# Kernel optimization log

Hardware: AMD Instinct MI355X
Metric: run time of the kernel (lower is better)

## Reference

```python
import jax, jax.numpy as jnp
import numpy as np

CUTOFFS = (2000, 20000, 50000)  # shortlist end, tail cluster boundaries; last == vocab
B, H, V = 8192, 1024, 50000
N_TAIL = len(CUTOFFS) - 1  # 2


def setup_inputs() -> dict:
    key = jax.random.key(0)
    ks = jax.random.split(key, 10)
    hidden = jax.random.normal(ks[0], (B, H), jnp.float32)
    targets = jax.random.randint(ks[1], (B,), 0, V, dtype=jnp.int64)
    embed_weight = jax.random.normal(ks[2], (V, H), jnp.float32) * 0.02
    # head: tail_vectors = nn.Linear(H, n_tail) -> W:(n_tail,H), b:(n_tail,)
    tail_vec_W = jax.random.normal(ks[3], (N_TAIL, H), jnp.float32) * 0.02
    tail_vec_b = jax.random.normal(ks[4], (N_TAIL,), jnp.float32) * 0.02
    shortlist_bias = jax.random.normal(ks[5], (CUTOFFS[0],), jnp.float32)
    bias0 = jax.random.normal(ks[6], (CUTOFFS[1] - CUTOFFS[0],), jnp.float32)
    bias1 = jax.random.normal(ks[7], (CUTOFFS[2] - CUTOFFS[1],), jnp.float32)
    # down_i = nn.Linear(H, H // 4**i, bias=False) -> W:(H//4**i, H)
    down0_W = jax.random.normal(ks[8], (H, H), jnp.float32) * (1.0 / np.sqrt(H))
    down1_W = jax.random.normal(ks[9], (H // 4, H), jnp.float32) * (1.0 / np.sqrt(H))
    return {
        "hidden": hidden, "embed_weight": embed_weight,
        "tail_vec_W": tail_vec_W, "tail_vec_b": tail_vec_b,
        "shortlist_bias": shortlist_bias, "bias0": bias0, "bias1": bias1,
        "down0_W": down0_W, "down1_W": down1_W, "targets": targets,
    }


def _cluster_ids(targets):
    # data-dependent sizes -> host-side index computation (matches torch nonzero)
    t = np.asarray(targets)
    ids = []
    for i in range(N_TAIL):
        ids.append(jnp.asarray(np.nonzero((t >= CUTOFFS[i]) & (t < CUTOFFS[i + 1]))[0]))
    return ids


def reference(hidden, embed_weight, tail_vec_W, tail_vec_b, shortlist_bias,
              bias0, bias1, down0_W, down1_W, targets):
    idx0, idx1 = _cluster_ids(targets)
    # head: shortlist logits + one logit per tail cluster
    shortlist = embed_weight[:CUTOFFS[0]]                       # (c0, H)
    head = jnp.concatenate(
        [hidden @ shortlist.T + shortlist_bias[None, :],         # (B, c0)
         hidden @ tail_vec_W.T + tail_vec_b[None, :]], axis=1)   # (B, n_tail)
    # tail cluster 0: down0 is H->H (reduce_factor**0 == 1, still applied)
    dec0 = embed_weight[CUTOFFS[0]:CUTOFFS[1]] @ down0_W.T       # (18000, H)
    out0 = (hidden[idx0] @ down0_W.T) @ dec0.T + bias0[None, :]  # (n0, 18000)
    # tail cluster 1: down1 is H -> H//4
    dec1 = embed_weight[CUTOFFS[1]:CUTOFFS[2]] @ down1_W.T       # (30000, 256)
    out1 = (hidden[idx1] @ down1_W.T) @ dec1.T + bias1[None, :]  # (n1, 30000)
    return (head, out0, out1)
```

## Files before the change

kernel.cpp:

```cpp
#include <hip/hip_runtime.h>
#include <hip/hip_bf16.h>

#define CUT0 2000
#define CUT1 20000
#define CUT2 50000
#define BSZ  8192
#define HDIM 1024
#define N0MAX 18000
#define N1MAX 30000
#define HEADW 2002

typedef __attribute__((ext_vector_type(8))) short bf16x8;
typedef __attribute__((ext_vector_type(4))) float f32x4;
typedef __attribute__((ext_vector_type(4))) unsigned short us4;

__device__ __forceinline__ unsigned short f2bf(float x) {
    unsigned u = __float_as_uint(x);
    unsigned r = u + 0x7fffu + ((u >> 16) & 1u);
    return (unsigned short)(r >> 16);
}

typedef const __attribute__((address_space(1))) void* gas_ptr;
typedef __attribute__((address_space(3))) void* las_ptr;

__device__ __forceinline__ void load_lds16(const void* g, void* l) {
    __builtin_amdgcn_global_load_lds((gas_ptr)g, (las_ptr)l, 16, 0, 0);
}

__global__ __launch_bounds__(1024) void build_idx(const int* __restrict__ targets,
                                                  int* __restrict__ n0,
                                                  int* __restrict__ n1,
                                                  int* __restrict__ idx0,
                                                  int* __restrict__ idx1) {
    __shared__ int s0[1024], s1[1024];
    const int t = threadIdx.x;
    const int base = t * 8;
    int tg[8];
    int c0 = 0, c1 = 0;
#pragma unroll
    for (int i = 0; i < 8; ++i) {
        tg[i] = targets[base + i];
        c0 += (tg[i] >= CUT0 && tg[i] < CUT1) ? 1 : 0;
        c1 += (tg[i] >= CUT1) ? 1 : 0;
    }
    s0[t] = c0; s1[t] = c1;
    __syncthreads();
    for (int off = 1; off < 1024; off <<= 1) {
        int v0 = 0, v1 = 0;
        if (t >= off) { v0 = s0[t - off]; v1 = s1[t - off]; }
        __syncthreads();
        s0[t] += v0; s1[t] += v1;
        __syncthreads();
    }
    int p0 = s0[t] - c0, p1 = s1[t] - c1;
#pragma unroll
    for (int i = 0; i < 8; ++i) {
        if (tg[i] >= CUT0 && tg[i] < CUT1)      idx0[p0++] = base + i;
        else if (tg[i] >= CUT1)                 idx1[p1++] = base + i;
    }
    if (t == 1023) { *n0 = s0[1023]; *n1 = s1[1023]; }
}

__global__ __launch_bounds__(256) void cvt_bf16(const float* __restrict__ src,
                                                unsigned short* __restrict__ dst,
                                                long long n) {
    long long i = ((long long)blockIdx.x * 256 + threadIdx.x) * 8;
    const long long stride = (long long)gridDim.x * 256 * 8;
    for (; i < n; i += stride) {
        f32x4 a = *(const f32x4*)(src + i);
        f32x4 b = *(const f32x4*)(src + i + 4);
        us4 p = { f2bf(a[0]), f2bf(a[1]), f2bf(a[2]), f2bf(a[3]) };
        us4 q = { f2bf(b[0]), f2bf(b[1]), f2bf(b[2]), f2bf(b[3]) };
        *(us4*)(dst + i)     = p;
        *(us4*)(dst + i + 4) = q;
    }
}

__global__ __launch_bounds__(256) void tail_head(const float* __restrict__ hidden,
                                                 const float* __restrict__ tailW,
                                                 const float* __restrict__ tailb,
                                                 float* __restrict__ out) {
    const int wave = threadIdx.x >> 6, lane = threadIdx.x & 63;
    const int row = blockIdx.x * 4 + wave;
    const float* h = hidden + (long long)row * HDIM;
    float s0 = 0.f, s1 = 0.f;
    for (int k = lane; k < HDIM; k += 64) {
        float x = h[k];
        s0 += x * tailW[k];
        s1 += x * tailW[HDIM + k];
    }
#pragma unroll
    for (int off = 32; off; off >>= 1) {
        s0 += __shfl_down(s0, off);
        s1 += __shfl_down(s1, off);
    }
    if (lane == 0) {
        out[(long long)row * HEADW + CUT0]     = s0 + tailb[0];
        out[(long long)row * HEADW + CUT0 + 1] = s1 + tailb[1];
    }
}

template<bool SPLIT_GATHER, bool OUT_BF16, bool HAS_BIAS>
__global__ __launch_bounds__(512) void gemm256(
    const unsigned short* __restrict__ A, const unsigned short* __restrict__ B,
    int gsplit, int gbase, const int* __restrict__ idxTail,
    int Mbase, const int* __restrict__ Mdev,
    int N, int K,
    const float* __restrict__ bias,
    void* __restrict__ Cv,
    long long coff, const int* __restrict__ coffM, long long coffScale,
    int ldC)
{
    const int M = Mbase + (Mdev ? *Mdev : 0);
    const int m0 = blockIdx.y * 256;
    const int n0 = blockIdx.x * 256;
    if (m0 >= M) return;

    __shared__ unsigned short As[4][8192];
    __shared__ unsigned short Bs[4][8192];

    const int tid  = threadIdx.x;
    const int wave = tid >> 6, lane = tid & 63;
    const int wr = wave >> 2;
    const int wc = wave & 3;
    const int lrow = lane & 15;
    const int quad = lane >> 4;

    const int srow = lane >> 2;
    const int scol = (((lane & 3) ^ (srow & 3)) << 3);

    int tr0 = wave * 32 + srow;
    int tr1 = tr0 + 16;

    int am0 = m0 + tr0; am0 = am0 < M ? am0 : M - 1;
    int am1 = m0 + tr1; am1 = am1 < M ? am1 : M - 1;
    long long ar0, ar1;
    if constexpr (SPLIT_GATHER) {
        ar0 = (am0 < gsplit) ? (long long)(gbase + am0) : (long long)idxTail[am0 - gsplit];
        ar1 = (am1 < gsplit) ? (long long)(gbase + am1) : (long long)idxTail[am1 - gsplit];
    } else {
        ar0 = am0; ar1 = am1;
    }
    const unsigned short* aP0 = A + ar0 * (long long)K + scol;
    const unsigned short* aP1 = A + ar1 * (long long)K + scol;

    int bn0 = n0 + tr0; bn0 = bn0 < N ? bn0 : N - 1;
    int bn1 = n0 + tr1; bn1 = bn1 < N ? bn1 : N - 1;
    const unsigned short* bP0 = B + (long long)bn0 * K + scol;
    const unsigned short* bP1 = B + (long long)bn1 * K + scol;

    f32x4 acc[8][4];
#pragma unroll
    for (int i = 0; i < 8; ++i)
#pragma unroll
        for (int j = 0; j < 4; ++j) acc[i][j] = (f32x4){0.f, 0.f, 0.f, 0.f};

    const int KT = K >> 5;

    auto issue = [&](int tt) {
        const int st = tt & 3;
        const int kofs = tt << 5;
        unsigned short* as = &As[st][wave * 1024];
        unsigned short* bs = &Bs[st][wave * 1024];
        load_lds16(aP0 + kofs, as);
        load_lds16(aP1 + kofs, as + 512);
        load_lds16(bP0 + kofs, bs);
        load_lds16(bP1 + kofs, bs + 512);
    };

    const int npro = KT < 3 ? KT : 3;
    for (int tt = 0; tt < npro; ++tt) issue(tt);

    const int rdswz = ((quad ^ (lrow & 3)) << 3);

    for (int t = 0; t < KT; ++t) {
        const int tt = t + 3;
        if (tt < KT) issue(tt);

        int infl = KT - 1 - t; if (infl > 3) infl = 3;
        if (infl >= 3)      asm volatile("s_waitcnt vmcnt(12)" ::: "memory");
        else if (infl == 2) asm volatile("s_waitcnt vmcnt(8)"  ::: "memory");
        else if (infl == 1) asm volatile("s_waitcnt vmcnt(4)"  ::: "memory");
        else                asm volatile("s_waitcnt vmcnt(0)"  ::: "memory");

        __builtin_amdgcn_s_barrier();
        asm volatile("" ::: "memory");

        const unsigned short* Asl = &As[t & 3][0];
        const unsigned short* Bsl = &Bs[t & 3][0];

        bf16x8 a[8], b[4];
#pragma unroll
        for (int mi = 0; mi < 8; ++mi) {
            const int R = wr * 128 + mi * 16 + lrow;
            a[mi] = *(const bf16x8*)&Asl[R * 32 + rdswz];
        }
#pragma unroll
        for (int nj = 0; nj < 4; ++nj) {
            const int R = wc * 64 + nj * 16 + lrow;
            b[nj] = *(const bf16x8*)&Bsl[R * 32 + rdswz];
        }

        __builtin_amdgcn_s_setprio(1);
#pragma unroll
        for (int mi = 0; mi < 8; ++mi)
#pragma unroll
            for (int nj = 0; nj < 4; ++nj)
                acc[mi][nj] = __builtin_amdgcn_mfma_f32_16x16x32_bf16(
                    a[mi], b[nj], acc[mi][nj], 0, 0, 0);
        __builtin_amdgcn_s_setprio(0);

        asm volatile("" ::: "memory");
        __builtin_amdgcn_s_barrier();
    }

    long long cbase = coff + (coffM ? (long long)(*coffM) * coffScale : 0ll);
#pragma unroll
    for (int mi = 0; mi < 8; ++mi) {
#pragma unroll
        for (int v = 0; v < 4; ++v) {
            int m = m0 + wr * 128 + mi * 16 + quad * 4 + v;
            if (m >= M) continue;
#pragma unroll
            for (int nj = 0; nj < 4; ++nj) {
                int n = n0 + wc * 64 + nj * 16 + lrow;
                if (n >= N) continue;
                float r = acc[mi][nj][v];
                if constexpr (OUT_BF16) {
                    ((unsigned short*)Cv)[(long long)m * ldC + n] = f2bf(r);
                } else {
                    if constexpr (HAS_BIAS) r += bias[n];
                    ((float*)Cv)[cbase + (long long)m * ldC + n] = r;
                }
            }
        }
    }
}

extern "C" void kernel_launch(void* const* d_in, const int* in_sizes, int n_in,
                              void* d_out, int out_size, void* d_ws, size_t ws_size,
                              hipStream_t stream) {
    (void)in_sizes; (void)n_in; (void)out_size; (void)ws_size;
    const float* hidden  = (const float*)d_in[0];
    const float* embed   = (const float*)d_in[1];
    const float* tailW   = (const float*)d_in[2];
    const float* tailb   = (const float*)d_in[3];
    const float* slbias  = (const float*)d_in[4];
    const float* bias0   = (const float*)d_in[5];
    const float* bias1   = (const float*)d_in[6];
    const float* down0   = (const float*)d_in[7];
    const float* down1   = (const float*)d_in[8];
    const int*   targets = (const int*)d_in[9];
    float* out = (float*)d_out;

    char* ws = (char*)d_ws;
    int* n0p  = (int*)ws;
    int* n1p  = n0p + 1;
    int* idx0 = (int*)(ws + 256);
    int* idx1 = idx0 + BSZ;
    size_t off = 256 + 2 * (size_t)BSZ * 4;
    unsigned short* ubf  = (unsigned short*)(ws + off);
    off += (size_t)(BSZ + CUT2) * HDIM * 2;
    unsigned short* c0   = (unsigned short*)(ws + off);
    off += (size_t)(N0MAX + BSZ) * HDIM * 2;
    unsigned short* c1   = (unsigned short*)(ws + off);
    off += (size_t)(N1MAX + BSZ) * 256 * 2;
    unsigned short* d0bf = (unsigned short*)(ws + off); off += (size_t)HDIM * HDIM * 2;
    unsigned short* d1bf = (unsigned short*)(ws + off); off += (size_t)256 * HDIM * 2;

    const unsigned short* ebf = ubf + (size_t)BSZ * HDIM;

    build_idx<<<1, 1024, 0, stream>>>(targets, n0p, n1p, idx0, idx1);

    cvt_bf16<<<2048, 256, 0, stream>>>(hidden, ubf, (long long)BSZ * HDIM);
    cvt_bf16<<<2048, 256, 0, stream>>>(embed,  (unsigned short*)ebf, (long long)CUT2 * HDIM);
    cvt_bf16<<<512,  256, 0, stream>>>(down0, d0bf, (long long)HDIM * HDIM);
    cvt_bf16<<<128,  256, 0, stream>>>(down1, d1bf, (long long)256 * HDIM);

    gemm256<false, false, true><<<dim3(8, 32), 512, 0, stream>>>(
        ubf, ebf, 0, 0, nullptr,
        BSZ, nullptr, CUT0, HDIM,
        slbias, out, 0ll, nullptr, 0ll, HEADW);

    tail_head<<<BSZ / 4, 256, 0, stream>>>(hidden, tailW, tailb, out);

    gemm256<true, true, false><<<dim3(4, 103), 512, 0, stream>>>(
        ubf, d0bf, N0MAX, BSZ + CUT0, idx0,
        N0MAX, n0p, HDIM, HDIM,
        nullptr, c0, 0ll, nullptr, 0ll, HDIM);

    gemm256<true, true, false><<<dim3(1, 150), 512, 0, stream>>>(
        ubf, d1bf, N1MAX, BSZ + CUT1, idx1,
        N1MAX, n1p, 256, HDIM,
        nullptr, c1, 0ll, nullptr, 0ll, 256);

    gemm256<false, false, true><<<dim3(71, 32), 512, 0, stream>>>(
        c0 + (size_t)N0MAX * HDIM, c0, 0, 0, nullptr,
        0, n0p, N0MAX, HDIM,
        bias0, out, (long long)BSZ * HEADW, nullptr, 0ll, N0MAX);

    gemm256<false, false, true><<<dim3(118, 32), 512, 0, stream>>>(
        c1 + (size_t)N1MAX * 256, c1, 0, 0, nullptr,
        0, n1p, N1MAX, 256,
        bias1, out, (long long)BSZ * HEADW, n0p, (long long)N0MAX, N1MAX);
}
```

Before: 1.667 ms.

## Fuse fp32-to-bf16 conversion of A operand into down-projection GEMMs, add XCD block remap

The down-projection GEMMs now read fp32 rows of embed or hidden directly, convert them to bf16 in registers and store them into LDS. This replaces the separate pass that converted all 48000 tail embedding rows to bf16, so only the 2000 shortlist rows still get a standalone conversion. The grids become 1D, and block IDs are remapped so that consecutive tiles land on the same XCD for better L2 locality. The cost is that register-staged A loads replace async global-to-LDS loads, adding VGPR pressure, LDS writes and an lgkmcnt wait in the pipeline.

```diff
diff --git a/kernel.cpp b/kernel.cpp
--- a/kernel.cpp
+++ b/kernel.cpp
@@ -18,6 +18,15 @@
     unsigned u = __float_as_uint(x);
     unsigned r = u + 0x7fffu + ((u >> 16) & 1u);
     return (unsigned short)(r >> 16);
+}
+
+__device__ __forceinline__ bf16x8 pack8(f32x4 a, f32x4 b) {
+    bf16x8 w;
+    w[0] = (short)f2bf(a[0]); w[1] = (short)f2bf(a[1]);
+    w[2] = (short)f2bf(a[2]); w[3] = (short)f2bf(a[3]);
+    w[4] = (short)f2bf(b[0]); w[5] = (short)f2bf(b[1]);
+    w[6] = (short)f2bf(b[2]); w[7] = (short)f2bf(b[3]);
+    return w;
 }
 
 typedef const __attribute__((address_space(1))) void* gas_ptr;
@@ -100,20 +109,28 @@
     }
 }
 
-template<bool SPLIT_GATHER, bool OUT_BF16, bool HAS_BIAS>
+template<bool A_F32, bool SPLIT_GATHER, bool OUT_BF16, bool HAS_BIAS>
 __global__ __launch_bounds__(512) void gemm256(
-    const unsigned short* __restrict__ A, const unsigned short* __restrict__ B,
+    const void* __restrict__ Av, const float* __restrict__ AgF,
+    const unsigned short* __restrict__ B,
     int gsplit, int gbase, const int* __restrict__ idxTail,
     int Mbase, const int* __restrict__ Mdev,
-    int N, int K,
+    int N, int K, int nbx,
     const float* __restrict__ bias,
     void* __restrict__ Cv,
     long long coff, const int* __restrict__ coffM, long long coffScale,
     int ldC)
 {
     const int M = Mbase + (Mdev ? *Mdev : 0);
-    const int m0 = blockIdx.y * 256;
-    const int n0 = blockIdx.x * 256;
+    int id = blockIdx.x;
+    {
+        const int nwg = (int)gridDim.x;
+        const int q = nwg >> 3, r = nwg & 7;
+        const int xcd = id & 7, pos = id >> 3;
+        id = (xcd < r ? xcd * (q + 1) : r * (q + 1) + (xcd - r) * q) + pos;
+    }
+    const int m0 = (id / nbx) * 256;
+    const int n0 = (id % nbx) * 256;
     if (m0 >= M) return;
 
     __shared__ unsigned short As[4][8192];
@@ -128,27 +145,43 @@
 
     const int srow = lane >> 2;
     const int scol = (((lane & 3) ^ (srow & 3)) << 3);
-
-    int tr0 = wave * 32 + srow;
-    int tr1 = tr0 + 16;
-
-    int am0 = m0 + tr0; am0 = am0 < M ? am0 : M - 1;
-    int am1 = m0 + tr1; am1 = am1 < M ? am1 : M - 1;
-    long long ar0, ar1;
-    if constexpr (SPLIT_GATHER) {
-        ar0 = (am0 < gsplit) ? (long long)(gbase + am0) : (long long)idxTail[am0 - gsplit];
-        ar1 = (am1 < gsplit) ? (long long)(gbase + am1) : (long long)idxTail[am1 - gsplit];
-    } else {
-        ar0 = am0; ar1 = am1;
-    }
-    const unsigned short* aP0 = A + ar0 * (long long)K + scol;
-    const unsigned short* aP1 = A + ar1 * (long long)K + scol;
-
+    int tr0 = wave * 32 + srow, tr1 = tr0 + 16;
     int bn0 = n0 + tr0; bn0 = bn0 < N ? bn0 : N - 1;
     int bn1 = n0 + tr1; bn1 = bn1 < N ? bn1 : N - 1;
     const unsigned short* bP0 = B + (long long)bn0 * K + scol;
     const unsigned short* bP1 = B + (long long)bn1 * K + scol;
 
+    const unsigned short* aP0 = nullptr;
+    const unsigned short* aP1 = nullptr;
+    const float* aF = nullptr;
+    int oA0 = 0, oA1 = 0, sA0 = 0, sA1 = 0;
+    if constexpr (!A_F32) {
+        int am0 = m0 + tr0; am0 = am0 < M ? am0 : M - 1;
+        int am1 = m0 + tr1; am1 = am1 < M ? am1 : M - 1;
+        long long ar0, ar1;
+        if constexpr (SPLIT_GATHER) {
+            ar0 = (am0 < gsplit) ? (long long)(gbase + am0) : (long long)idxTail[am0 - gsplit];
+            ar1 = (am1 < gsplit) ? (long long)(gbase + am1) : (long long)idxTail[am1 - gsplit];
+        } else { ar0 = am0; ar1 = am1; }
+        const unsigned short* Ab = (const unsigned short*)Av;
+        aP0 = Ab + ar0 * (long long)K + scol;
+        aP1 = Ab + ar1 * (long long)K + scol;
+    } else {
+        const int rA  = lane >> 1;
+        const int trA = wave * 32 + rA;
+        int amF = m0 + trA; amF = amF < M ? amF : M - 1;
+        long long rowi; const float* bp;
+        if constexpr (SPLIT_GATHER) {
+            if (amF < gsplit) { rowi = (long long)(gbase + amF); bp = (const float*)Av; }
+            else              { rowi = (long long)idxTail[amF - gsplit]; bp = AgF; }
+        } else { rowi = amF; bp = (const float*)Av; }
+        aF  = bp + rowi * (long long)K;
+        sA0 = (lane & 1);
+        sA1 = 2 + (lane & 1);
+        oA0 = trA * 32 + ((sA0 ^ (trA & 3)) << 3);
+        oA1 = trA * 32 + ((sA1 ^ (trA & 3)) << 3);
+    }
+
     f32x4 acc[8][4];
 #pragma unroll
     for (int i = 0; i < 8; ++i)
@@ -157,31 +190,67 @@
 
     const int KT = K >> 5;
 
-    auto issue = [&](int tt) {
-        const int st = tt & 3;
-        const int kofs = tt << 5;
-        unsigned short* as = &As[st][wave * 1024];
-        unsigned short* bs = &Bs[st][wave * 1024];
-        load_lds16(aP0 + kofs, as);
-        load_lds16(aP1 + kofs, as + 512);
-        load_lds16(bP0 + kofs, bs);
-        load_lds16(bP1 + kofs, bs + 512);
+    auto issueB = [&](int tt) {
+        unsigned short* bs = &Bs[tt & 3][wave * 1024];
+        load_lds16(bP0 + (tt << 5), bs);
+        load_lds16(bP1 + (tt << 5), bs + 512);
     };
+    auto issueA16 = [&](int tt) {
+        unsigned short* as = &As[tt & 3][wave * 1024];
+        load_lds16(aP0 + (tt << 5), as);
+        load_lds16(aP1 + (tt << 5), as + 512);
+    };
 
     const int npro = KT < 3 ? KT : 3;
-    for (int tt = 0; tt < npro; ++tt) issue(tt);
+    for (int tt = 0; tt < npro; ++tt) {
+        issueB(tt);
+        if constexpr (!A_F32) {
+            issueA16(tt);
+        } else {
+            const float* p = aF + (tt << 5);
+            f32x4 x0 = *(const f32x4*)(p + sA0 * 8);
+            f32x4 x1 = *(const f32x4*)(p + sA0 * 8 + 4);
+            f32x4 y0 = *(const f32x4*)(p + sA1 * 8);
+            f32x4 y1 = *(const f32x4*)(p + sA1 * 8 + 4);
+            *(bf16x8*)&As[tt & 3][oA0] = pack8(x0, x1);
+            *(bf16x8*)&As[tt & 3][oA1] = pack8(y0, y1);
+        }
+    }
+    if constexpr (A_F32)
+        asm volatile("s_waitcnt lgkmcnt(0)" ::: "memory");
 
     const int rdswz = ((quad ^ (lrow & 3)) << 3);
 
     for (int t = 0; t < KT; ++t) {
         const int tt = t + 3;
-        if (tt < KT) issue(tt);
+        const bool pf = (tt < KT);
+
+        f32x4 x0, x1, y0, y1;
+        if constexpr (!A_F32) {
+            if (pf) { issueB(tt); issueA16(tt); }
+        } else {
+            if (pf) {
+                issueB(tt);
+                const float* p = aF + (tt << 5);
+                x0 = *(const f32x4*)(p + sA0 * 8);
+                x1 = *(const f32x4*)(p + sA0 * 8 + 4);
+                y0 = *(const f32x4*)(p + sA1 * 8);
+                y1 = *(const f32x4*)(p + sA1 * 8 + 4);
+            }
+        }
 
         int infl = KT - 1 - t; if (infl > 3) infl = 3;
-        if (infl >= 3)      asm volatile("s_waitcnt vmcnt(12)" ::: "memory");
-        else if (infl == 2) asm volatile("s_waitcnt vmcnt(8)"  ::: "memory");
-        else if (infl == 1) asm volatile("s_waitcnt vmcnt(4)"  ::: "memory");
-        else                asm volatile("s_waitcnt vmcnt(0)"  ::: "memory");
+        if constexpr (!A_F32) {
+            if (infl >= 3)      asm volatile("s_waitcnt vmcnt(12)" ::: "memory");
+            else if (infl == 2) asm volatile("s_waitcnt vmcnt(8)"  ::: "memory");
+            else if (infl == 1) asm volatile("s_waitcnt vmcnt(4)"  ::: "memory");
+            else                asm volatile("s_waitcnt vmcnt(0)"  ::: "memory");
+        } else {
+            if (infl >= 3)      asm volatile("s_waitcnt vmcnt(10)" ::: "memory");
+            else if (infl == 2) asm volatile("s_waitcnt vmcnt(4)"  ::: "memory");
+            else if (infl == 1) asm volatile("s_waitcnt vmcnt(2)"  ::: "memory");
+            else                asm volatile("s_waitcnt vmcnt(0)"  ::: "memory");
+        }
 
         __builtin_amdgcn_s_barrier();
         asm volatile("" ::: "memory");
@@ -209,6 +278,14 @@
                 acc[mi][nj] = __builtin_amdgcn_mfma_f32_16x16x32_bf16(
                     a[mi], b[nj], acc[mi][nj], 0, 0, 0);
         __builtin_amdgcn_s_setprio(0);
+
+        if constexpr (A_F32) {
+            if (pf) {
+                *(bf16x8*)&As[tt & 3][oA0] = pack8(x0, x1);
+                *(bf16x8*)&As[tt & 3][oA1] = pack8(y0, y1);
+            }
+            asm volatile("s_waitcnt lgkmcnt(0)" ::: "memory");
+        }
 
         asm volatile("" ::: "memory");
         __builtin_amdgcn_s_barrier();
@@ -259,8 +336,8 @@
     int* idx0 = (int*)(ws + 256);
     int* idx1 = idx0 + BSZ;
     size_t off = 256 + 2 * (size_t)BSZ * 4;
-    unsigned short* ubf  = (unsigned short*)(ws + off);
-    off += (size_t)(BSZ + CUT2) * HDIM * 2;
+    unsigned short* hbf  = (unsigned short*)(ws + off); off += (size_t)BSZ * HDIM * 2;
+    unsigned short* ebf  = (unsigned short*)(ws + off); off += (size_t)CUT0 * HDIM * 2;
     unsigned short* c0   = (unsigned short*)(ws + off);
     off += (size_t)(N0MAX + BSZ) * HDIM * 2;
     unsigned short* c1   = (unsigned short*)(ws + off);
@@ -268,39 +345,37 @@
     unsigned short* d0bf = (unsigned short*)(ws + off); off += (size_t)HDIM * HDIM * 2;
     unsigned short* d1bf = (unsigned short*)(ws + off); off += (size_t)256 * HDIM * 2;
 
-    const unsigned short* ebf = ubf + (size_t)BSZ * HDIM;
-
     build_idx<<<1, 1024, 0, stream>>>(targets, n0p, n1p, idx0, idx1);
 
-    cvt_bf16<<<2048, 256, 0, stream>>>(hidden, ubf, (long long)BSZ * HDIM);
-    cvt_bf16<<<2048, 256, 0, stream>>>(embed,  (unsigned short*)ebf, (long long)CUT2 * HDIM);
+    cvt_bf16<<<2048, 256, 0, stream>>>(hidden, hbf, (long long)BSZ * HDIM);
+    cvt_bf16<<<512,  256, 0, stream>>>(embed,  ebf, (long long)CUT0 * HDIM);
     cvt_bf16<<<512,  256, 0, stream>>>(down0, d0bf, (long long)HDIM * HDIM);
     cvt_bf16<<<128,  256, 0, stream>>>(down1, d1bf, (long long)256 * HDIM);
 
-    gemm256<false, false, true><<<dim3(8, 32), 512, 0, stream>>>(
-        ubf, ebf, 0, 0, nullptr,
-        BSZ, nullptr, CUT0, HDIM,
+    gemm256<false, false, false, true><<<8 * 32, 512, 0, stream>>>(
+        hbf, nullptr, ebf, 0, 0, nullptr,
+        BSZ, nullptr, CUT0, HDIM, 8,
         slbias, out, 0ll, nullptr, 0ll, HEADW);
 
     tail_head<<<BSZ / 4, 256, 0, stream>>>(hidden, tailW, tailb, out);
 
-    gemm256<true, true, false><<<dim3(4, 103), 512, 0, stream>>>(
-        ubf, d0bf, N0MAX, BSZ + CUT0, idx0,
-        N0MAX, n0p, HDIM, HDIM,
+    gemm256<true, true, true, false><<<4 * 103, 512, 0, stream>>>(
+        embed, hidden, d0bf, N0MAX, CUT0, idx0,
+        N0MAX, n0p, HDIM, HDIM, 4,
         nullptr, c0, 0ll, nullptr, 0ll, HDIM);
 
-    gemm256<true, true, false><<<dim3(1, 150), 512, 0, stream>>>(
-        ubf, d1bf, N1MAX, BSZ + CUT1, idx1,
-        N1MAX, n1p, 256, HDIM,
+    gemm256<true, true, true, false><<<1 * 150, 512, 0, stream>>>(
+        embed, hidden, d1bf, N1MAX, CUT1, idx1,
+        N1MAX, n1p, 256, HDIM, 1,
         nullptr, c1, 0ll, nullptr, 0ll, 256);
 
-    gemm256<false, false, true><<<dim3(71, 32), 512, 0, stream>>>(
-        c0 + (size_t)N0MAX * HDIM, c0, 0, 0, nullptr,
-        0, n0p, N0MAX, HDIM,
+    gemm256<false, false, false, true><<<71 * 32, 512, 0, stream>>>(
+        c0 + (size_t)N0MAX * HDIM, nullptr, c0, 0, 0, nullptr,
+        0, n0p, N0MAX, HDIM, 71,
         bias0, out, (long long)BSZ * HEADW, nullptr, 0ll, N0MAX);
 
-    gemm256<false, false, true><<<dim3(118, 32), 512, 0, stream>>>(
-        c1 + (size_t)N1MAX * 256, c1, 0, 0, nullptr,
-        0, n1p, N1MAX, 256,
+    gemm256<false, false, false, true><<<118 * 32, 512, 0, stream>>>(
+        c1 + (size_t)N1MAX * 256, nullptr, c1, 0, 0, nullptr,
+        0, n1p, N1MAX, 256, 118,
         bias1, out, (long long)BSZ * HEADW, n0p, (long long)N0MAX, N1MAX);
 }
```

Result: slower. 2.098 ms (+25.8%).
